# Optimization experiments

Measured on AMD Instinct MI355X. Metric: run time of the kernel, lower is better.

The kernel has to match this reference:

```python
import jax, jax.numpy as jnp
import numpy as np

N_ORDER = 256
DT = 1.0 / 4096.0


def _hippo_legs(N):
    # legs measure transition matrices (float64 numpy, matches torch module)
    q = np.arange(N, dtype=np.float64)
    col, row = np.meshgrid(q, q)
    r = 2 * q + 1
    M = -(np.where(row >= col, r, 0) - np.diag(q))
    T = np.sqrt(np.diag(2 * q + 1))
    A = T @ M @ np.linalg.inv(T)
    B = np.diag(T)[:, None].copy()
    return A, B


def _bilinear_discretize(A, B, dt):
    # scipy cont2discrete 'bilinear' (Tustin): dA = (I - dt/2 A)^-1 (I + dt/2 A), dB = (I - dt/2 A)^-1 dt B
    N = A.shape[0]
    I = np.eye(N)
    M = np.linalg.inv(I - (dt / 2.0) * A)
    dA = M @ (I + (dt / 2.0) * A)
    dB = (M @ (dt * B)).squeeze(-1)
    # module rounds to 7 decimals
    return np.round(dA, decimals=7), np.round(dB, decimals=7)


def setup_inputs() -> dict:
    key = jax.random.key(0)
    inputs = jax.random.normal(key, (4096, 64), dtype=jnp.float32)
    A, B = _hippo_legs(N_ORDER)  # c=0.0 so no diagonal shift
    dA, dB = _bilinear_discretize(A, B, DT)
    return {
        "inputs": inputs,
        "dA": jnp.asarray(dA, dtype=jnp.float32),  # (N, N)
        "dB": jnp.asarray(dB, dtype=jnp.float32),  # (N,)
    }


def reference(inputs, dA, dB):
    # inputs: (L, B) -> output (L, B, N)
    # recurrence: c_t = c_{t-1} @ dA^T + dB * u_t
    u = inputs[..., None] * dB  # (L, B, N)

    def step(c, u_t):
        c = c @ dA.T + u_t
        return c, c

    c0 = jnp.zeros(u.shape[1:], dtype=u.dtype)
    _, cs = jax.lax.scan(step, c0, u)
    return cs
```

## Files before the change

kernel.cpp:

```cpp
#include <hip/hip_runtime.h>
#include <math.h>


#define L_SEQ 4096
#define BATCH 64
#define NST   256
#define NCH   32
#define CLEN  128
#define RSTR  20

template<int CTRL, int RMASK>
__device__ __forceinline__ float dpp_mov_f(float x, float ident) {
  union { float f; int i; } a, b, r;
  a.f = x; b.f = ident;
  r.i = __builtin_amdgcn_update_dpp(b.i, a.i, CTRL, RMASK, 0xF, false);
  return r.f;
}

__device__ __forceinline__ float wave_iscan_add(float v) {
  v += dpp_mov_f<0x111, 0xF>(v, 0.f);
  v += dpp_mov_f<0x112, 0xF>(v, 0.f);
  v += dpp_mov_f<0x114, 0xF>(v, 0.f);
  v += dpp_mov_f<0x118, 0xF>(v, 0.f);
  v += dpp_mov_f<0x142, 0xA>(v, 0.f);
  v += dpp_mov_f<0x143, 0xC>(v, 0.f);
  return v;
}

template<int CTRL, int RMASK>
__device__ __forceinline__ double dpp_mov_d(double x, double ident) {
  union { double d; int i[2]; } a, b, r;
  a.d = x; b.d = ident;
  r.i[0] = __builtin_amdgcn_update_dpp(b.i[0], a.i[0], CTRL, RMASK, 0xF, false);
  r.i[1] = __builtin_amdgcn_update_dpp(b.i[1], a.i[1], CTRL, RMASK, 0xF, false);
  return r.d;
}

__device__ __forceinline__ double wave_iscan_mul(double v) {
  v *= dpp_mov_d<0x111, 0xF>(v, 1.0);
  v *= dpp_mov_d<0x112, 0xF>(v, 1.0);
  v *= dpp_mov_d<0x114, 0xF>(v, 1.0);
  v *= dpp_mov_d<0x118, 0xF>(v, 1.0);
  v *= dpp_mov_d<0x142, 0xA>(v, 1.0);
  v *= dpp_mov_d<0x143, 0xC>(v, 1.0);
  return v;
}

__device__ __forceinline__ void compute_params(int lane, const float* __restrict__ dA,
                                               float d[4], float p[4], float q[4]) {
  const double delta = 1.0 / 8192.0;
  double D[4], g[4];
  #pragma unroll
  for (int m = 0; m < 4; ++m) {
    int n = 4 * lane + m;
    D[m] = 1.0 + delta * (double)(n + 1);
    g[m] = 1.0 - delta * (double)(2 * n + 1) / D[m];
  }
  double h01  = g[0] * g[1];
  double h012 = h01 * g[2];
  double h    = h012 * g[3];
  double incl = wave_iscan_mul(h);
  double excl = incl / h;
  double Wm1[4];
  Wm1[0] = excl;
  Wm1[1] = excl * g[0];
  Wm1[2] = excl * h01;
  Wm1[3] = excl * h012;
  #pragma unroll
  for (int m = 0; m < 4; ++m) {
    int n = 4 * lane + m;
    double r = sqrt(2.0 * (double)n + 1.0);
    double W = Wm1[m] * g[m];
    p[m] = (float)(-2.0 * (delta * r / D[m]) * Wm1[m]);
    q[m] = (float)((r / D[m]) / W);
    d[m] = dA[n * NST + n];
  }
}

__device__ __forceinline__ void hippo_step(float& c0, float& c1, float& c2, float& c3,
                                           const float d[4], const float p[4], const float q[4],
                                           float i0, float i1, float i2, float i3) {
  float qc0 = q[0] * c0, qc1 = q[1] * c1, qc2 = q[2] * c2, qc3 = q[3] * c3;
  float t01 = qc0 + qc1, t23 = qc2 + qc3, tot = t01 + t23;
  float s  = wave_iscan_add(tot);
  float e0 = s - tot;
  float e1 = e0 + qc0, e2 = e0 + t01, e3 = e2 + qc2;
  c0 = fmaf(d[0], c0, fmaf(p[0], e0, i0));
  c1 = fmaf(d[1], c1, fmaf(p[1], e1, i1));
  c2 = fmaf(d[2], c2, fmaf(p[2], e2, i2));
  c3 = fmaf(d[3], c3, fmaf(p[3], e3, i3));
}

__device__ __forceinline__ float bcast_lane(float v, int l) {
  return __int_as_float(__builtin_amdgcn_readlane(__float_as_int(v), l));
}

__device__ __forceinline__ size_t inc_addr(int k, int b) {
  return ((size_t)(k * CLEN) * BATCH + b) * NST;
}
__device__ __forceinline__ size_t f_addr(int k, int b) {
  return ((size_t)(k * CLEN + 1) * BATCH + b) * NST;
}
__device__ __forceinline__ size_t mt_addr(int j) {
  return ((size_t)((j >> 6) * CLEN + 2) * BATCH + (j & 63)) * NST;
}

__global__ __launch_bounds__(256) void k_pass1(const float* __restrict__ u,
                                               const float* __restrict__ dA,
                                               const float* __restrict__ dB,
                                               float* __restrict__ out) {
  int wid  = blockIdx.x * 4 + (threadIdx.x >> 6);
  int lane = threadIdx.x & 63;
  float d[4], p[4], q[4];
  compute_params(lane, dA, d, p, q);
  float c0 = 0.f, c1 = 0.f, c2 = 0.f, c3 = 0.f;
  if (wid < NCH * BATCH) {
    int k = wid >> 6, b = wid & 63;
    float4 db = *reinterpret_cast<const float4*>(dB + 4 * lane);
    for (int half = 0; half < CLEN / 64; ++half) {
      float ur = u[(size_t)(k * CLEN + half * 64 + lane) * BATCH + b];
      #pragma unroll 4
      for (int i = 0; i < 64; ++i) {
        float uv = bcast_lane(ur, i);
        hippo_step(c0, c1, c2, c3, d, p, q,
                   db.x * uv, db.y * uv, db.z * uv, db.w * uv);
      }
    }
    *reinterpret_cast<float4*>(out + f_addr(k, b) + 4 * lane) =
        make_float4(c0, c1, c2, c3);
  } else {
    int j = wid - NCH * BATCH;
    c0 = (4 * lane + 0 == j) ? 1.f : 0.f;
    c1 = (4 * lane + 1 == j) ? 1.f : 0.f;
    c2 = (4 * lane + 2 == j) ? 1.f : 0.f;
    c3 = (4 * lane + 3 == j) ? 1.f : 0.f;
    #pragma unroll 4
    for (int i = 0; i < CLEN; ++i)
      hippo_step(c0, c1, c2, c3, d, p, q, 0.f, 0.f, 0.f, 0.f);
    *reinterpret_cast<float4*>(out + mt_addr(j) + 4 * lane) =
        make_float4(c0, c1, c2, c3);
  }
}

__global__ __launch_bounds__(256) void k_passB(float* __restrict__ out) {
  int bg   = blockIdx.x;
  int tid  = threadIdx.x;
  int w    = tid >> 6, l = tid & 63;
  __shared__ float xs[NST * 4];
  __shared__ float red[4 * 64 * RSTR];

  *reinterpret_cast<float4*>(&xs[tid * 4]) = make_float4(0.f, 0.f, 0.f, 0.f);
  #pragma unroll
  for (int bb = 0; bb < 4; ++bb)
    out[inc_addr(0, 4 * bg + bb) + tid] = 0.f;
  __syncthreads();

  for (int k = 1; k < NCH; ++k) {
    float4 a0 = make_float4(0.f, 0.f, 0.f, 0.f);
    float4 a1 = a0, a2 = a0, a3 = a0;
    #pragma unroll 8
    for (int j0 = 0; j0 < 64; ++j0) {
      int j = w * 64 + j0;
      float4 col = *reinterpret_cast<const float4*>(out + mt_addr(j) + 4 * l);
      float4 x4  = *reinterpret_cast<const float4*>(&xs[j * 4]);
      a0.x = fmaf(col.x, x4.x, a0.x); a0.y = fmaf(col.y, x4.x, a0.y);
      a0.z = fmaf(col.z, x4.x, a0.z); a0.w = fmaf(col.w, x4.x, a0.w);
      a1.x = fmaf(col.x, x4.y, a1.x); a1.y = fmaf(col.y, x4.y, a1.y);
      a1.z = fmaf(col.z, x4.y, a1.z); a1.w = fmaf(col.w, x4.y, a1.w);
      a2.x = fmaf(col.x, x4.z, a2.x); a2.y = fmaf(col.y, x4.z, a2.y);
      a2.z = fmaf(col.z, x4.z, a2.z); a2.w = fmaf(col.w, x4.z, a2.w);
      a3.x = fmaf(col.x, x4.w, a3.x); a3.y = fmaf(col.y, x4.w, a3.y);
      a3.z = fmaf(col.z, x4.w, a3.z); a3.w = fmaf(col.w, x4.w, a3.w);
    }
    float* rb = &red[(w * 64 + l) * RSTR];
    *reinterpret_cast<float4*>(rb + 0)  = a0;
    *reinterpret_cast<float4*>(rb + 4)  = a1;
    *reinterpret_cast<float4*>(rb + 8)  = a2;
    *reinterpret_cast<float4*>(rb + 12) = a3;
    __syncthreads();
    int b = 4 * bg + w;
    float4 y = *reinterpret_cast<const float4*>(out + f_addr(k - 1, b) + 4 * l);
    #pragma unroll
    for (int wp = 0; wp < 4; ++wp) {
      float4 r4 = *reinterpret_cast<const float4*>(&red[(wp * 64 + l) * RSTR + w * 4]);
      y.x += r4.x; y.y += r4.y; y.z += r4.z; y.w += r4.w;
    }
    *reinterpret_cast<float4*>(out + inc_addr(k, b) + 4 * l) = y;
    xs[(4 * l + 0) * 4 + w] = y.x;
    xs[(4 * l + 1) * 4 + w] = y.y;
    xs[(4 * l + 2) * 4 + w] = y.z;
    xs[(4 * l + 3) * 4 + w] = y.w;
    __syncthreads();
  }
}

__global__ __launch_bounds__(256) void k_pass3(const float* __restrict__ u,
                                               const float* __restrict__ dA,
                                               const float* __restrict__ dB,
                                               float* __restrict__ out) {
  int wid  = blockIdx.x * 4 + (threadIdx.x >> 6);
  int lane = threadIdx.x & 63;
  int k = wid >> 6, b = wid & 63;
  float d[4], p[4], q[4];
  compute_params(lane, dA, d, p, q);
  float4 db = *reinterpret_cast<const float4*>(dB + 4 * lane);
  size_t oa = inc_addr(k, b) + 4 * lane;
  float4 c = *reinterpret_cast<const float4*>(out + oa);
  float c0 = c.x, c1 = c.y, c2 = c.z, c3 = c.w;
  for (int half = 0; half < CLEN / 64; ++half) {
    float ur = u[(size_t)(k * CLEN + half * 64 + lane) * BATCH + b];
    #pragma unroll 4
    for (int i = 0; i < 64; ++i) {
      float uv = bcast_lane(ur, i);
      hippo_step(c0, c1, c2, c3, d, p, q,
                 db.x * uv, db.y * uv, db.z * uv, db.w * uv);
      *reinterpret_cast<float4*>(out + oa) = make_float4(c0, c1, c2, c3);
      oa += (size_t)BATCH * NST;
    }
  }
}

extern "C" void kernel_launch(void* const* d_in, const int* in_sizes, int n_in,
                              void* d_out, int out_size, void* d_ws, size_t ws_size,
                              hipStream_t stream) {
  const float* u  = (const float*)d_in[0];
  const float* dA = (const float*)d_in[1];
  const float* dB = (const float*)d_in[2];
  float* out = (float*)d_out;
  (void)in_sizes; (void)n_in; (void)out_size; (void)d_ws; (void)ws_size;

  k_pass1<<<(NCH * BATCH + NST) / 4, 256, 0, stream>>>(u, dA, dB, out);
  k_passB<<<BATCH / 4, 256, 0, stream>>>(out);
  k_pass3<<<(NCH * BATCH) / 4, 256, 0, stream>>>(u, dA, dB, out);
}
```

Measured before the change: 393.3 us.

## Fuse three HiPPO passes into one cooperative kernel with grid syncs

Merges the chunk-local scan, the serial cross-chunk carry propagation and the final rescan into one cooperative kernel, separated by grid-wide syncs. This removes the launch gaps between the three kernels. The carry stage now gives one block to each batch element (64 blocks instead of 16), with wave 0 doing the reduction, so the serial 31-step chain has more parallelism. The final output stream uses nontemporal stores. The trade-offs are the cost of the grid-wide barriers, an occupancy hint of 3 blocks per CU needed for co-residency, and most blocks sitting idle during the carry stage.

```diff
diff --git a/kernel.cpp b/kernel.cpp
--- a/kernel.cpp
+++ b/kernel.cpp
@@ -1,5 +1,8 @@
 #include <hip/hip_runtime.h>
+#include <hip/hip_cooperative_groups.h>
 #include <math.h>
+
+namespace cg = cooperative_groups;
 
 
 #define L_SEQ 4096
@@ -7,7 +10,9 @@
 #define NST   256
 #define NCH   32
 #define CLEN  128
-#define RSTR  20
+#define NBLK  576
+
+typedef float fx4 __attribute__((ext_vector_type(4)));
 
 template<int CTRL, int RMASK>
 __device__ __forceinline__ float dpp_mov_f(float x, float ident) {
@@ -105,18 +110,96 @@
   return ((size_t)((j >> 6) * CLEN + 2) * BATCH + (j & 63)) * NST;
 }
 
-__global__ __launch_bounds__(256) void k_pass1(const float* __restrict__ u,
-                                               const float* __restrict__ dA,
-                                               const float* __restrict__ dB,
-                                               float* __restrict__ out) {
-  int wid  = blockIdx.x * 4 + (threadIdx.x >> 6);
-  int lane = threadIdx.x & 63;
+__global__ __launch_bounds__(256, 3) void k_fused(const float* __restrict__ u,
+                                                  const float* __restrict__ dA,
+                                                  const float* __restrict__ dB,
+                                                  float* __restrict__ out) {
+  cg::grid_group grid = cg::this_grid();
+  const int tid  = threadIdx.x;
+  const int w    = tid >> 6;
+  const int lane = tid & 63;
+  const int wid  = blockIdx.x * 4 + w;
+
+  __shared__ float xs[NST];
+  __shared__ float red[256 * 5];
+
   float d[4], p[4], q[4];
   compute_params(lane, dA, d, p, q);
-  float c0 = 0.f, c1 = 0.f, c2 = 0.f, c3 = 0.f;
+
+  {
+    float c0 = 0.f, c1 = 0.f, c2 = 0.f, c3 = 0.f;
+    if (wid < NCH * BATCH) {
+      int k = wid >> 6, b = wid & 63;
+      float4 db = *reinterpret_cast<const float4*>(dB + 4 * lane);
+      for (int half = 0; half < CLEN / 64; ++half) {
+        float ur = u[(size_t)(k * CLEN + half * 64 + lane) * BATCH + b];
+        #pragma unroll 4
+        for (int i = 0; i < 64; ++i) {
+          float uv = bcast_lane(ur, i);
+          hippo_step(c0, c1, c2, c3, d, p, q,
+                     db.x * uv, db.y * uv, db.z * uv, db.w * uv);
+        }
+      }
+      *reinterpret_cast<float4*>(out + f_addr(k, b) + 4 * lane) =
+          make_float4(c0, c1, c2, c3);
+    } else {
+      int j = wid - NCH * BATCH;
+      c0 = (4 * lane + 0 == j) ? 1.f : 0.f;
+      c1 = (4 * lane + 1 == j) ? 1.f : 0.f;
+      c2 = (4 * lane + 2 == j) ? 1.f : 0.f;
+      c3 = (4 * lane + 3 == j) ? 1.f : 0.f;
+      #pragma unroll 4
+      for (int i = 0; i < CLEN; ++i)
+        hippo_step(c0, c1, c2, c3, d, p, q, 0.f, 0.f, 0.f, 0.f);
+      *reinterpret_cast<float4*>(out + mt_addr(j) + 4 * lane) =
+          make_float4(c0, c1, c2, c3);
+    }
+  }
+
+  grid.sync();
+
+  if (blockIdx.x < BATCH) {
+    const int b = blockIdx.x;
+    xs[tid] = 0.f;
+    out[inc_addr(0, b) + tid] = 0.f;
+    __syncthreads();
+    for (int k = 1; k < NCH; ++k) {
+      float ax = 0.f, ay = 0.f, az = 0.f, aw = 0.f;
+      #pragma unroll 8
+      for (int j0 = 0; j0 < 64; ++j0) {
+        int j = w * 64 + j0;
+        float4 col = *reinterpret_cast<const float4*>(out + mt_addr(j) + 4 * lane);
+        float x = xs[j];
+        ax = fmaf(col.x, x, ax); ay = fmaf(col.y, x, ay);
+        az = fmaf(col.z, x, az); aw = fmaf(col.w, x, aw);
+      }
+      int idx = (w * 64 + lane) * 5;
+      red[idx + 0] = ax; red[idx + 1] = ay;
+      red[idx + 2] = az; red[idx + 3] = aw;
+      __syncthreads();
+      if (w == 0) {
+        float4 y = *reinterpret_cast<const float4*>(out + f_addr(k - 1, b) + 4 * lane);
+        #pragma unroll
+        for (int wp = 0; wp < 4; ++wp) {
+          int ri = (wp * 64 + lane) * 5;
+          y.x += red[ri + 0]; y.y += red[ri + 1];
+          y.z += red[ri + 2]; y.w += red[ri + 3];
+        }
+        *reinterpret_cast<float4*>(out + inc_addr(k, b) + 4 * lane) = y;
+        *reinterpret_cast<float4*>(&xs[4 * lane]) = y;
+      }
+      __syncthreads();
+    }
+  }
+
+  grid.sync();
+
   if (wid < NCH * BATCH) {
     int k = wid >> 6, b = wid & 63;
     float4 db = *reinterpret_cast<const float4*>(dB + 4 * lane);
+    size_t oa = inc_addr(k, b) + 4 * lane;
+    float4 c = *reinterpret_cast<const float4*>(out + oa);
+    float c0 = c.x, c1 = c.y, c2 = c.z, c3 = c.w;
     for (int half = 0; half < CLEN / 64; ++half) {
       float ur = u[(size_t)(k * CLEN + half * 64 + lane) * BATCH + b];
       #pragma unroll 4
@@ -124,98 +207,10 @@
         float uv = bcast_lane(ur, i);
         hippo_step(c0, c1, c2, c3, d, p, q,
                    db.x * uv, db.y * uv, db.z * uv, db.w * uv);
-      }
-    }
-    *reinterpret_cast<float4*>(out + f_addr(k, b) + 4 * lane) =
-        make_float4(c0, c1, c2, c3);
-  } else {
-    int j = wid - NCH * BATCH;
-    c0 = (4 * lane + 0 == j) ? 1.f : 0.f;
-    c1 = (4 * lane + 1 == j) ? 1.f : 0.f;
-    c2 = (4 * lane + 2 == j) ? 1.f : 0.f;
-    c3 = (4 * lane + 3 == j) ? 1.f : 0.f;
-    #pragma unroll 4
-    for (int i = 0; i < CLEN; ++i)
-      hippo_step(c0, c1, c2, c3, d, p, q, 0.f, 0.f, 0.f, 0.f);
-    *reinterpret_cast<float4*>(out + mt_addr(j) + 4 * lane) =
-        make_float4(c0, c1, c2, c3);
-  }
-}
-
-__global__ __launch_bounds__(256) void k_passB(float* __restrict__ out) {
-  int bg   = blockIdx.x;
-  int tid  = threadIdx.x;
-  int w    = tid >> 6, l = tid & 63;
-  __shared__ float xs[NST * 4];
-  __shared__ float red[4 * 64 * RSTR];
-
-  *reinterpret_cast<float4*>(&xs[tid * 4]) = make_float4(0.f, 0.f, 0.f, 0.f);
-  #pragma unroll
-  for (int bb = 0; bb < 4; ++bb)
-    out[inc_addr(0, 4 * bg + bb) + tid] = 0.f;
-  __syncthreads();
-
-  for (int k = 1; k < NCH; ++k) {
-    float4 a0 = make_float4(0.f, 0.f, 0.f, 0.f);
-    float4 a1 = a0, a2 = a0, a3 = a0;
-    #pragma unroll 8
-    for (int j0 = 0; j0 < 64; ++j0) {
-      int j = w * 64 + j0;
-      float4 col = *reinterpret_cast<const float4*>(out + mt_addr(j) + 4 * l);
-      float4 x4  = *reinterpret_cast<const float4*>(&xs[j * 4]);
-      a0.x = fmaf(col.x, x4.x, a0.x); a0.y = fmaf(col.y, x4.x, a0.y);
-      a0.z = fmaf(col.z, x4.x, a0.z); a0.w = fmaf(col.w, x4.x, a0.w);
-      a1.x = fmaf(col.x, x4.y, a1.x); a1.y = fmaf(col.y, x4.y, a1.y);
-      a1.z = fmaf(col.z, x4.y, a1.z); a1.w = fmaf(col.w, x4.y, a1.w);
-      a2.x = fmaf(col.x, x4.z, a2.x); a2.y = fmaf(col.y, x4.z, a2.y);
-      a2.z = fmaf(col.z, x4.z, a2.z); a2.w = fmaf(col.w, x4.z, a2.w);
-      a3.x = fmaf(col.x, x4.w, a3.x); a3.y = fmaf(col.y, x4.w, a3.y);
-      a3.z = fmaf(col.z, x4.w, a3.z); a3.w = fmaf(col.w, x4.w, a3.w);
-    }
-    float* rb = &red[(w * 64 + l) * RSTR];
-    *reinterpret_cast<float4*>(rb + 0)  = a0;
-    *reinterpret_cast<float4*>(rb + 4)  = a1;
-    *reinterpret_cast<float4*>(rb + 8)  = a2;
-    *reinterpret_cast<float4*>(rb + 12) = a3;
-    __syncthreads();
-    int b = 4 * bg + w;
-    float4 y = *reinterpret_cast<const float4*>(out + f_addr(k - 1, b) + 4 * l);
-    #pragma unroll
-    for (int wp = 0; wp < 4; ++wp) {
-      float4 r4 = *reinterpret_cast<const float4*>(&red[(wp * 64 + l) * RSTR + w * 4]);
-      y.x += r4.x; y.y += r4.y; y.z += r4.z; y.w += r4.w;
-    }
-    *reinterpret_cast<float4*>(out + inc_addr(k, b) + 4 * l) = y;
-    xs[(4 * l + 0) * 4 + w] = y.x;
-    xs[(4 * l + 1) * 4 + w] = y.y;
-    xs[(4 * l + 2) * 4 + w] = y.z;
-    xs[(4 * l + 3) * 4 + w] = y.w;
-    __syncthreads();
-  }
-}
-
-__global__ __launch_bounds__(256) void k_pass3(const float* __restrict__ u,
-                                               const float* __restrict__ dA,
-                                               const float* __restrict__ dB,
-                                               float* __restrict__ out) {
-  int wid  = blockIdx.x * 4 + (threadIdx.x >> 6);
-  int lane = threadIdx.x & 63;
-  int k = wid >> 6, b = wid & 63;
-  float d[4], p[4], q[4];
-  compute_params(lane, dA, d, p, q);
-  float4 db = *reinterpret_cast<const float4*>(dB + 4 * lane);
-  size_t oa = inc_addr(k, b) + 4 * lane;
-  float4 c = *reinterpret_cast<const float4*>(out + oa);
-  float c0 = c.x, c1 = c.y, c2 = c.z, c3 = c.w;
-  for (int half = 0; half < CLEN / 64; ++half) {
-    float ur = u[(size_t)(k * CLEN + half * 64 + lane) * BATCH + b];
-    #pragma unroll 4
-    for (int i = 0; i < 64; ++i) {
-      float uv = bcast_lane(ur, i);
-      hippo_step(c0, c1, c2, c3, d, p, q,
-                 db.x * uv, db.y * uv, db.z * uv, db.w * uv);
-      *reinterpret_cast<float4*>(out + oa) = make_float4(c0, c1, c2, c3);
-      oa += (size_t)BATCH * NST;
+        fx4 v; v.x = c0; v.y = c1; v.z = c2; v.w = c3;
+        __builtin_nontemporal_store(v, reinterpret_cast<fx4*>(out + oa));
+        oa += (size_t)BATCH * NST;
+      }
     }
   }
 }
@@ -229,7 +224,7 @@
   float* out = (float*)d_out;
   (void)in_sizes; (void)n_in; (void)out_size; (void)d_ws; (void)ws_size;
 
-  k_pass1<<<(NCH * BATCH + NST) / 4, 256, 0, stream>>>(u, dA, dB, out);
-  k_passB<<<BATCH / 4, 256, 0, stream>>>(out);
-  k_pass3<<<(NCH * BATCH) / 4, 256, 0, stream>>>(u, dA, dB, out);
-}
+  void* args[] = {(void*)&u, (void*)&dA, (void*)&dB, (void*)&out};
+  hipLaunchCooperativeKernel((const void*)k_fused, dim3(NBLK), dim3(256),
+                             args, 0, stream);
+}
```

Result: slower. 518.9 us (+31.9%).
